# Optimization experiments

Measured on AMD Instinct MI355X. Metric: run time of the kernel, lower is better.

## Reference

```python
import jax, jax.numpy as jnp
import numpy as np

N, E, D = 50000, 800000, 128
RESIDUAL_SCALE = 1.0
EPS = 1e-5  # torch LayerNorm default eps


def _mlp_ln(h, w1, b1, w2, b2, w3, b3, g, beta):
    # MeshGraphNets MLP: Linear -> SiLU -> Linear -> SiLU -> Linear -> LayerNorm
    h = jax.nn.silu(h @ w1 + b1)
    h = jax.nn.silu(h @ w2 + b2)
    h = h @ w3 + b3
    mu = h.mean(axis=-1, keepdims=True)
    var = ((h - mu) ** 2).mean(axis=-1, keepdims=True)
    return g * (h - mu) * jax.lax.rsqrt(var + EPS) + beta


def setup_inputs() -> dict:
    key = jax.random.key(0)
    ks = jax.random.split(key, 16)

    def lin(k, fan_in, fan_out):
        bound = 1.0 / np.sqrt(fan_in)
        kw, kb = jax.random.split(k)
        w = jax.random.uniform(kw, (fan_in, fan_out), jnp.float32, -bound, bound)
        b = jax.random.uniform(kb, (fan_out,), jnp.float32, -bound, bound)
        return w, b

    x = jax.random.normal(ks[0], (N, D), jnp.float32)
    edge_attr = jax.random.normal(ks[1], (E, D), jnp.float32)
    edge_index = jax.random.randint(ks[2], (2, E), 0, N, jnp.int32)

    ew1, eb1 = lin(ks[3], 3 * D, D)
    ew2, eb2 = lin(ks[4], D, D)
    ew3, eb3 = lin(ks[5], D, D)
    e_gamma = jnp.ones((D,), jnp.float32)
    e_beta = jnp.zeros((D,), jnp.float32)

    nw1, nb1 = lin(ks[6], 2 * D, D)
    nw2, nb2 = lin(ks[7], D, D)
    nw3, nb3 = lin(ks[8], D, D)
    n_gamma = jnp.ones((D,), jnp.float32)
    n_beta = jnp.zeros((D,), jnp.float32)

    return dict(x=x, edge_attr=edge_attr, edge_index=edge_index,
                ew1=ew1, eb1=eb1, ew2=ew2, eb2=eb2, ew3=ew3, eb3=eb3,
                e_gamma=e_gamma, e_beta=e_beta,
                nw1=nw1, nb1=nb1, nw2=nw2, nb2=nb2, nw3=nw3, nb3=nb3,
                n_gamma=n_gamma, n_beta=n_beta)


def reference(x, edge_attr, edge_index,
              ew1, eb1, ew2, eb2, ew3, eb3, e_gamma, e_beta,
              nw1, nb1, nw2, nb2, nw3, nb3, n_gamma, n_beta):
    senders, receivers = edge_index[0], edge_index[1]

    # EdgeBlock: gather endpoint node features, concat with edge_attr, MLP
    edge_in = jnp.concatenate([x[senders], x[receivers], edge_attr], axis=-1)  # [E, 3D]
    edge_mlp_out = _mlp_ln(edge_in, ew1, eb1, ew2, eb2, ew3, eb3, e_gamma, e_beta)  # [E, D]

    # NodeBlock: scatter-sum edge messages to receiver nodes, concat with x, MLP
    agg = jax.ops.segment_sum(edge_mlp_out, receivers, num_segments=N)  # [N, D]
    node_in = jnp.concatenate([x, agg], axis=-1)  # [N, 2D]
    node_mlp_out = _mlp_ln(node_in, nw1, nb1, nw2, nb2, nw3, nb3, n_gamma, n_beta)

    # Residual updates
    x_new = x + RESIDUAL_SCALE * node_mlp_out

    # PairNorm (use_pairnorm=True)
    x_centered = x_new - x_new.mean(axis=0, keepdims=True)
    rms = jnp.linalg.norm(x_centered) / jnp.sqrt(jnp.float32(x_new.shape[0])) + 1e-8
    x_new = x_centered / rms

    edge_attr_new = edge_attr + RESIDUAL_SCALE * edge_mlp_out
    return x_new, edge_attr_new
```

## Files before the change

### kernel.cpp

```cpp
#include <hip/hip_runtime.h>
#include <hip/hip_bf16.h>

#define NN 50000
#define NE 800000
#define ROWB 272

typedef unsigned short u16;
typedef unsigned int u32;
typedef __attribute__((ext_vector_type(4))) float f32x4;
typedef __attribute__((ext_vector_type(8))) short short8;


__device__ __forceinline__ u16 f2b(float f){ __hip_bfloat16 h = __float2bfloat16(f); u16 u; __builtin_memcpy(&u, &h, 2); return u; }
__device__ __forceinline__ float b2f(u16 u){ __hip_bfloat16 h; __builtin_memcpy(&h, &u, 2); return __bfloat162float(h); }
__device__ __forceinline__ float siluf(float v){ return v / (1.f + __expf(-v)); }

__device__ __forceinline__ uint4 cvt8(const float* __restrict__ s){
  const float4 a = *(const float4*)s;
  const float4 b = *(const float4*)(s + 4);
  union { u16 h[8]; uint4 q; } u;
  u.h[0]=f2b(a.x); u.h[1]=f2b(a.y); u.h[2]=f2b(a.z); u.h[3]=f2b(a.w);
  u.h[4]=f2b(b.x); u.h[5]=f2b(b.y); u.h[6]=f2b(b.z); u.h[7]=f2b(b.w);
  return u.q;
}

template<int K>
__device__ __forceinline__ void gemm128(f32x4 acc[4][2], const u16* __restrict__ sA,
                                        const u16* __restrict__ wB, int wm, int wn, int lane){
  const int l15 = lane & 15, l4 = lane >> 4;
  const u16* w0 = wB + (size_t)(wn*32 + l15)*K + l4*8;
  const u16* w1 = w0 + (size_t)16*K;
  #pragma unroll
  for (int ks = 0; ks < 4; ++ks){
    const short8 b0 = *(const short8*)(w0 + ks*32);
    const short8 b1 = *(const short8*)(w1 + ks*32);
    const int kb = ks*64 + l4*16;
    short8 a[4];
    #pragma unroll
    for (int fr = 0; fr < 4; ++fr)
      a[fr] = *(const short8*)((const char*)sA + (wm*64 + fr*16 + l15)*ROWB + kb);
    #pragma unroll
    for (int fr = 0; fr < 4; ++fr){
      acc[fr][0] = __builtin_amdgcn_mfma_f32_16x16x32_bf16(a[fr], b0, acc[fr][0], 0, 0, 0);
      acc[fr][1] = __builtin_amdgcn_mfma_f32_16x16x32_bf16(a[fr], b1, acc[fr][1], 0, 0, 0);
    }
  }
}

template<int K>
__device__ __forceinline__ void gemm64(f32x4 acc[2][4], const u16* __restrict__ sA,
                                       const u16* __restrict__ wB, int wm, int wn, int lane){
  const int l15 = lane & 15, l4 = lane >> 4;
  const u16* w0 = wB + (size_t)(wn*64 + l15)*K + l4*8;
  #pragma unroll
  for (int ks = 0; ks < 4; ++ks){
    short8 b[4];
    #pragma unroll
    for (int fc = 0; fc < 4; ++fc)
      b[fc] = *(const short8*)(w0 + (size_t)fc*16*K + ks*32);
    const int kb = ks*64 + l4*16;
    short8 a[2];
    #pragma unroll
    for (int fr = 0; fr < 2; ++fr)
      a[fr] = *(const short8*)((const char*)sA + (wm*32 + fr*16 + l15)*ROWB + kb);
    #pragma unroll
    for (int fr = 0; fr < 2; ++fr)
      #pragma unroll
      for (int fc = 0; fc < 4; ++fc)
        acc[fr][fc] = __builtin_amdgcn_mfma_f32_16x16x32_bf16(a[fr], b[fc], acc[fr][fc], 0, 0, 0);
  }
}

__device__ __forceinline__ void epilogue(const f32x4 acc[4][2], const float* __restrict__ bias,
                                         u16* __restrict__ dst, int wm, int wn, int lane, bool doSilu){
  const int l15 = lane & 15, l4 = lane >> 4;
  #pragma unroll
  for (int fc = 0; fc < 2; ++fc){
    const int col = wn*32 + fc*16 + l15;
    const float bv = bias[col];
    #pragma unroll
    for (int fr = 0; fr < 4; ++fr){
      const int rbase = wm*64 + fr*16 + l4*4;
      #pragma unroll
      for (int j = 0; j < 4; ++j){
        float v = acc[fr][fc][j] + bv;
        if (doSilu) v = siluf(v);
        *(u16*)((char*)dst + (rbase + j)*ROWB + col*2) = f2b(v);
      }
    }
  }
}

__global__ __launch_bounds__(256) void prep_kernel(const float* __restrict__ w1, const float* __restrict__ w2,
                                                   const float* __restrict__ w3, const float* __restrict__ m1,
                                                   const float* __restrict__ m2, const float* __restrict__ m3,
                                                   u16* __restrict__ wt,
                                                   const float* __restrict__ x, u16* __restrict__ xB,
                                                   const int* __restrict__ eidx, int* __restrict__ cnt){
  const int i = blockIdx.x * 256 + threadIdx.x;
  if (i < 147456){
    const float* src; int K, base, off;
    if      (i < 49152)  { src = w1; K = 384; base = 0;      off = i; }
    else if (i < 65536)  { src = w2; K = 128; base = 49152;  off = i - 49152; }
    else if (i < 81920)  { src = w3; K = 128; base = 65536;  off = i - 65536; }
    else if (i < 114688) { src = m1; K = 256; base = 81920;  off = i - 81920; }
    else if (i < 131072) { src = m2; K = 128; base = 114688; off = i - 114688; }
    else                 { src = m3; K = 128; base = 131072; off = i - 131072; }
    const int k = off >> 7, n = off & 127;
    wt[base + n*K + k] = f2b(src[off]);
  }
  if (xB){
    const size_t o = (size_t)i * 8;
    *(uint4*)(xB + o) = cvt8(x + o);
  }
  atomicAdd(&cnt[eidx[NE + i]], 1);
}

__global__ __launch_bounds__(1024) void scan_kernel(const int* __restrict__ cnt, int* __restrict__ off,
                                                    int* __restrict__ cursor){
  __shared__ int s[1024];
  const int t = threadIdx.x;
  const int CH = 49;
  int sum = 0;
  for (int i = 0; i < CH; ++i){
    const int idx = t*CH + i;
    if (idx < NN) sum += cnt[idx];
  }
  s[t] = sum;
  __syncthreads();
  for (int d = 1; d < 1024; d <<= 1){
    int v = (t >= d) ? s[t - d] : 0;
    __syncthreads();
    s[t] += v;
    __syncthreads();
  }
  int run = s[t] - sum;
  for (int i = 0; i < CH; ++i){
    const int idx = t*CH + i;
    if (idx < NN){
      off[idx] = run;
      cursor[idx] = run;
      run += cnt[idx];
      if (idx == NN - 1) off[NN] = run;
    }
  }
}

__global__ __launch_bounds__(256) void scatter_kernel(const int* __restrict__ eidx, int* __restrict__ cursor,
                                                      int* __restrict__ perm, int* __restrict__ slot){
  const int i = blockIdx.x * 256 + threadIdx.x;
  if (i < NE){
    const int pos = atomicAdd(&cursor[eidx[NE + i]], 1);
    perm[pos] = i;
    slot[i] = pos;
  }
}

__global__ __launch_bounds__(256, 4) void pre_kernel(const float* __restrict__ x, const u16* __restrict__ xB,
                                                     const u16* __restrict__ wt, u16* __restrict__ Pab){
  __shared__ u16 sX[64*136];
  const int t = threadIdx.x;
  const int nBase = blockIdx.x * 64;
  const int lane = t & 63, wid = t >> 6;
  const int wm = wid >> 1, wn = wid & 1;
  const int chunk = t & 15, r0 = t >> 4;

  #pragma unroll
  for (int p = 0; p < 4; ++p){
    const int row = r0 + p*16;
    const int node = nBase + row;
    uint4 v = {0u, 0u, 0u, 0u};
    if (node < NN){
      if (xB) v = *(const uint4*)(xB + (size_t)node*128 + chunk*8);
      else    v = cvt8(x + (size_t)node*128 + chunk*8);
    }
    *(uint4*)((char*)sX + row*ROWB + chunk*16) = v;
  }
  __syncthreads();

  const f32x4 z4 = {0.f, 0.f, 0.f, 0.f};
  const int l15 = lane & 15, l4 = lane >> 4;
  #pragma unroll
  for (int half = 0; half < 2; ++half){
    f32x4 acc[2][4];
    #pragma unroll
    for (int fr = 0; fr < 2; ++fr)
      #pragma unroll
      for (int fc = 0; fc < 4; ++fc) acc[fr][fc] = z4;
    gemm64<384>(acc, sX, wt + half*128, wm, wn, lane);
    #pragma unroll
    for (int fc = 0; fc < 4; ++fc){
      const int col = wn*64 + fc*16 + l15;
      #pragma unroll
      for (int fr = 0; fr < 2; ++fr){
        const int rbase = wm*32 + fr*16 + l4*4;
        #pragma unroll
        for (int j = 0; j < 4; ++j){
          const int node = nBase + rbase + j;
          if (node < NN) Pab[(size_t)node*256 + half*128 + col] = f2b(acc[fr][fc][j]);
        }
      }
    }
  }
}

__global__ __launch_bounds__(512, 4) void edge_kernel(
    const float* __restrict__ ea, const int* __restrict__ eidx,
    const u16* __restrict__ wt, const u16* __restrict__ Pab,
    const float* __restrict__ b1, const float* __restrict__ b2,
    const float* __restrict__ b3, const float* __restrict__ gma, const float* __restrict__ bta,
    const int* __restrict__ slot, float* __restrict__ outE, u16* __restrict__ oBuf)
{
  __shared__ u16 sA[128*136];
  __shared__ float sMeta[640];
  __shared__ int sIdx[256];
  __shared__ int sSlot[128];
  const int t = threadIdx.x;
  const size_t eBase = (size_t)blockIdx.x * 128;

  if (t < 128){
    sIdx[t]       = eidx[eBase + t];
    sIdx[t + 128] = eidx[(size_t)NE + eBase + t];
    sSlot[t]      = slot[eBase + t];
    sMeta[t]       = b1[t];
    sMeta[t + 128] = b2[t];
    sMeta[t + 256] = b3[t];
    sMeta[t + 384] = gma[t];
    sMeta[t + 512] = bta[t];
  }
  __syncthreads();

  const int lane = t & 63, wid = t >> 6;
  const int wm = wid >> 2, wn = wid & 3;
  const int chunk = t & 15, r0 = t >> 4;
  const int l15 = lane & 15, l4 = lane >> 4;

  #pragma unroll
  for (int p = 0; p < 4; ++p){
    const int row = r0 + p*32;
    const int sn = sIdx[row], rn = sIdx[row + 128];
    const uint4 qa = *(const uint4*)(Pab + (size_t)sn*256 + chunk*8);
    const uint4 qb = *(const uint4*)(Pab + (size_t)rn*256 + 128 + chunk*8);
    const u16* pa = (const u16*)&qa;
    const u16* pb = (const u16*)&qb;
    union { u16 h[8]; uint4 q; } u;
    #pragma unroll
    for (int j = 0; j < 8; ++j) u.h[j] = f2b(b2f(pa[j]) + b2f(pb[j]));
    *(uint4*)((char*)sA + row*ROWB + chunk*16) = u.q;
  }
  __syncthreads();

  f32x4 acc[4][2];
  #pragma unroll
  for (int fr = 0; fr < 4; ++fr)
    #pragma unroll
    for (int fc = 0; fc < 2; ++fc){
      const int col = wn*32 + fc*16 + l15;
      #pragma unroll
      for (int j = 0; j < 4; ++j)
        acc[fr][fc][j] = b2f(*(const u16*)((const char*)sA + (wm*64 + fr*16 + l4*4 + j)*ROWB + col*2));
    }
  __syncthreads();

  uint4 eaQ[4];
  #pragma unroll
  for (int p = 0; p < 4; ++p){
    const int row = r0 + p*32;
    uint4 v = cvt8(ea + ((eBase + row)*128 + chunk*8));
    eaQ[p] = v;
    *(uint4*)((char*)sA + row*ROWB + chunk*16) = v;
  }
  __syncthreads();
  gemm128<384>(acc, sA, wt + 256, wm, wn, lane);
  __syncthreads();
  epilogue(acc, sMeta + 0, sA, wm, wn, lane, true);
  __syncthreads();
  const f32x4 z4 = {0.f, 0.f, 0.f, 0.f};
  #pragma unroll
  for (int fr = 0; fr < 4; ++fr){ acc[fr][0] = z4; acc[fr][1] = z4; }
  gemm128<128>(acc, sA, wt + 49152, wm, wn, lane);
  __syncthreads();
  epilogue(acc, sMeta + 128, sA, wm, wn, lane, true);
  __syncthreads();
  #pragma unroll
  for (int fr = 0; fr < 4; ++fr){ acc[fr][0] = z4; acc[fr][1] = z4; }
  gemm128<128>(acc, sA, wt + 65536, wm, wn, lane);
  __syncthreads();
  epilogue(acc, sMeta + 256, sA, wm, wn, lane, false);
  __syncthreads();

  {
    #pragma unroll
    for (int p = 0; p < 4; ++p){
      const int row = r0 + p*32;
      uint4 q = *(const uint4*)((const char*)sA + row*ROWB + chunk*16);
      const u16* pu = (const u16*)&q;
      float h[8];
      #pragma unroll
      for (int j = 0; j < 8; ++j) h[j] = b2f(pu[j]);
      float s = 0.f;
      #pragma unroll
      for (int j = 0; j < 8; ++j) s += h[j];
      s += __shfl_xor(s, 1); s += __shfl_xor(s, 2); s += __shfl_xor(s, 4); s += __shfl_xor(s, 8);
      const float mu = s * (1.f/128.f);
      float ss = 0.f;
      #pragma unroll
      for (int j = 0; j < 8; ++j){ const float d = h[j] - mu; ss += d*d; }
      ss += __shfl_xor(ss, 1); ss += __shfl_xor(ss, 2); ss += __shfl_xor(ss, 4); ss += __shfl_xor(ss, 8);
      const float rs = rsqrtf(fmaxf(ss*(1.f/128.f), 0.f) + 1e-5f);
      const size_t e = eBase + row;
      const u16* ep = (const u16*)&eaQ[p];
      alignas(16) float orow[8];
      alignas(16) u16 obf[8];
      #pragma unroll
      for (int j = 0; j < 8; ++j){
        const int col = chunk*8 + j;
        const float o = sMeta[384 + col]*(h[j] - mu)*rs + sMeta[512 + col];
        orow[j] = b2f(ep[j]) + o;
        obf[j] = f2b(o);
      }
      float* dst = outE + e*128 + chunk*8;
      *(float4*)dst       = ((const float4*)orow)[0];
      *(float4*)(dst + 4) = ((const float4*)orow)[1];
      if (oBuf) *(uint4*)(oBuf + (size_t)sSlot[row]*128 + chunk*8) = *(const uint4*)obf;
    }
  }
}

__global__ __launch_bounds__(256) void agg_f_kernel(const float* __restrict__ outE, const float* __restrict__ ea,
                                                    const int* __restrict__ off, const int* __restrict__ perm,
                                                    float* __restrict__ agg){
  const int node = blockIdx.x * 4 + (threadIdx.x >> 6);
  const int lane = threadIdx.x & 63;
  if (node >= NN) return;
  const int s = off[node], e = off[node + 1];
  float a0 = 0.f, a1 = 0.f;
  for (int i = s; i < e; ++i){
    const size_t r = (size_t)perm[i] * 128;
    a0 += outE[r + lane]      - ea[r + lane];
    a1 += outE[r + 64 + lane] - ea[r + 64 + lane];
  }
  agg[(size_t)node*128 + lane]      = a0;
  agg[(size_t)node*128 + 64 + lane] = a1;
}

__global__ __launch_bounds__(512, 4) void node_kernel(
    const float* __restrict__ x, const float* __restrict__ aggF,
    const u16* __restrict__ oBuf, const int* __restrict__ off,
    const u16* __restrict__ wt,
    const float* __restrict__ b1, const float* __restrict__ b2, const float* __restrict__ b3,
    const float* __restrict__ gma, const float* __restrict__ bta,
    float* __restrict__ outX, float* __restrict__ stats)
{
  __shared__ u16 sA[128*136];
  __shared__ float sMeta[640];
  __shared__ float sCol[128];
  __shared__ float sSq;
  const int t = threadIdx.x;
  const int nBase = blockIdx.x * 128;

  if (t < 128){
    sMeta[t]       = b1[t];
    sMeta[t + 128] = b2[t];
    sMeta[t + 256] = b3[t];
    sMeta[t + 384] = gma[t];
    sMeta[t + 512] = bta[t];
    sCol[t] = 0.f;
  }
  if (t == 0) sSq = 0.f;
  __syncthreads();

  const int lane = t & 63, wid = t >> 6;
  const int wm = wid >> 2, wn = wid & 3;
  const int chunk = t & 15, r0 = t >> 4;

  const f32x4 z4 = {0.f, 0.f, 0.f, 0.f};
  f32x4 acc[4][2];
  #pragma unroll
  for (int fr = 0; fr < 4; ++fr){ acc[fr][0] = z4; acc[fr][1] = z4; }

  for (int kc = 0; kc < 2; ++kc){
    #pragma unroll
    for (int p = 0; p < 4; ++p){
      const int row = r0 + p*32;
      const int node = nBase + row;
      uint4 v = {0u, 0u, 0u, 0u};
      if (node < NN){
        if (kc == 0){
          v = cvt8(x + (size_t)node*128 + chunk*8);
        } else if (oBuf){
          float a[8] = {0.f,0.f,0.f,0.f,0.f,0.f,0.f,0.f};
          const int s0 = off[node], e0 = off[node + 1];
          for (int i = s0; i < e0; ++i){
            uint4 q = *(const uint4*)(oBuf + (size_t)i*128 + chunk*8);
            const u16* pu = (const u16*)&q;
            #pragma unroll
            for (int j = 0; j < 8; ++j) a[j] += b2f(pu[j]);
          }
          union { u16 h[8]; uint4 q; } u;
          #pragma unroll
          for (int j = 0; j < 8; ++j) u.h[j] = f2b(a[j]);
          v = u.q;
        } else {
          v = cvt8(aggF + (size_t)node*128 + chunk*8);
        }
      }
      *(uint4*)((char*)sA + row*ROWB + chunk*16) = v;
    }
    __syncthreads();
    gemm128<256>(acc, sA, wt + 81920 + kc*128, wm, wn, lane);
    __syncthreads();
  }
  epilogue(acc, sMeta + 0, sA, wm, wn, lane, true);
  __syncthreads();
  #pragma unroll
  for (int fr = 0; fr < 4; ++fr){ acc[fr][0] = z4; acc[fr][1] = z4; }
  gemm128<128>(acc, sA, wt + 114688, wm, wn, lane);
  __syncthreads();
  epilogue(acc, sMeta + 128, sA, wm, wn, lane, true);
  __syncthreads();
  #pragma unroll
  for (int fr = 0; fr < 4; ++fr){ acc[fr][0] = z4; acc[fr][1] = z4; }
  gemm128<128>(acc, sA, wt + 131072, wm, wn, lane);
  __syncthreads();
  epilogue(acc, sMeta + 256, sA, wm, wn, lane, false);
  __syncthreads();

  {
    const int row = t >> 2, part = t & 3;
    const int node = nBase + row;
    float v[32];
    #pragma unroll
    for (int c = 0; c < 4; ++c){
      uint4 q = *(const uint4*)((const char*)sA + row*ROWB + part*64 + c*16);
      const u16* pu = (const u16*)&q;
      #pragma unroll
      for (int j = 0; j < 8; ++j) v[c*8 + j] = b2f(pu[j]);
    }
    float s = 0.f;
    #pragma unroll
    for (int i = 0; i < 32; ++i) s += v[i];
    s += __shfl_xor(s, 1);  s += __shfl_xor(s, 2);
    const float mu = s * (1.f/128.f);
    float ss = 0.f;
    #pragma unroll
    for (int i = 0; i < 32; ++i){ const float d = v[i] - mu; ss += d*d; }
    ss += __shfl_xor(ss, 1);  ss += __shfl_xor(ss, 2);
    const float rs = rsqrtf(fmaxf(ss*(1.f/128.f), 0.f) + 1e-5f);
    float lssq = 0.f;
    if (node < NN){
      const float* xRow = x + (size_t)node*128 + part*32;
      alignas(16) float orow[32];
      #pragma unroll
      for (int i = 0; i < 32; ++i){
        const int col = part*32 + i;
        const float o = sMeta[384 + col]*(v[i] - mu)*rs + sMeta[512 + col];
        const float res = xRow[i] + o;
        orow[i] = res;
        atomicAdd(&sCol[col], res);
        lssq += res*res;
      }
      float* dst = outX + (size_t)node*128 + part*32;
      #pragma unroll
      for (int c = 0; c < 8; ++c) *(float4*)(dst + c*4) = ((const float4*)orow)[c];
    }
    #pragma unroll
    for (int m = 1; m < 64; m <<= 1) lssq += __shfl_xor(lssq, m);
    if (lane == 0) atomicAdd(&sSq, lssq);
  }
  __syncthreads();
  if (t < 128) atomicAdd(&stats[t], sCol[t]);
  if (t == 0)  atomicAdd(&stats[128], sSq);
}

__global__ __launch_bounds__(256) void pairnorm_kernel(float* __restrict__ xOut, const float* __restrict__ stats){
  __shared__ float sMean[128];
  __shared__ float sP2[2];
  __shared__ float sInv;
  const int t = threadIdx.x;
  float m2 = 0.f;
  if (t < 128){
    const float mean = stats[t] * (1.f / (float)NN);
    sMean[t] = mean;
    m2 = mean * mean;
  }
  #pragma unroll
  for (int m = 1; m < 64; m <<= 1) m2 += __shfl_xor(m2, m);
  if ((t & 63) == 0 && t < 128) sP2[t >> 6] = m2;
  __syncthreads();
  if (t == 0){
    float ssc = stats[128] - (float)NN * (sP2[0] + sP2[1]);
    ssc = fmaxf(ssc, 0.f);
    const float rms = sqrtf(ssc * (1.f / (float)NN)) + 1e-8f;
    sInv = 1.f / rms;
  }
  __syncthreads();
  const size_t base = ((size_t)blockIdx.x * 256 + t) * 4;
  const int col = (int)(base & 127);
  float4 q = *(float4*)(xOut + base);
  const float inv = sInv;
  q.x = (q.x - sMean[col])     * inv;
  q.y = (q.y - sMean[col + 1]) * inv;
  q.z = (q.z - sMean[col + 2]) * inv;
  q.w = (q.w - sMean[col + 3]) * inv;
  *(float4*)(xOut + base) = q;
}

extern "C" void kernel_launch(void* const* d_in, const int* in_sizes, int n_in,
                              void* d_out, int out_size, void* d_ws, size_t ws_size,
                              hipStream_t stream){
  (void)in_sizes; (void)n_in; (void)out_size;
  const float* x    = (const float*)d_in[0];
  const float* ea   = (const float*)d_in[1];
  const int*   eidx = (const int*)d_in[2];
  const float* ew1  = (const float*)d_in[3];
  const float* eb1  = (const float*)d_in[4];
  const float* ew2  = (const float*)d_in[5];
  const float* eb2  = (const float*)d_in[6];
  const float* ew3  = (const float*)d_in[7];
  const float* eb3  = (const float*)d_in[8];
  const float* eg   = (const float*)d_in[9];
  const float* ebt  = (const float*)d_in[10];
  const float* nw1  = (const float*)d_in[11];
  const float* nb1  = (const float*)d_in[12];
  const float* nw2  = (const float*)d_in[13];
  const float* nb2  = (const float*)d_in[14];
  const float* nw3  = (const float*)d_in[15];
  const float* nb3  = (const float*)d_in[16];
  const float* ng   = (const float*)d_in[17];
  const float* nbt  = (const float*)d_in[18];

  u16*   wt     = (u16*)d_ws;
  float* stats  = (float*)((char*)d_ws + 294912);
  int*   cnt    = (int*)((char*)d_ws + 297216);
  int*   off    = (int*)((char*)d_ws + 497408);
  int*   cursor = (int*)((char*)d_ws + 697600);
  int*   perm   = (int*)((char*)d_ws + 897792);
  int*   slot   = (int*)((char*)d_ws + 4097792);
  const bool useO = ws_size >= (7297792ull + (size_t)NE * 128 * 2);
  const bool useX = ws_size >= (7297792ull + (size_t)NE * 128 * 2 + (size_t)NN * 128 * 2);
  u16*   oBuf   = useO ? (u16*)((char*)d_ws + 7297792) : (u16*)nullptr;
  u16*   xB     = useX ? (u16*)((char*)d_ws + 7297792 + (size_t)NE * 128 * 2) : (u16*)nullptr;
  float* outX   = (float*)d_out;
  u16*   Pab    = (u16*)d_out;
  float* outE   = outX + (size_t)NN * 128;

  hipMemsetAsync(stats, 0, 2048, stream);
  hipMemsetAsync(cnt, 0, NN * sizeof(int), stream);
  prep_kernel<<<3125, 256, 0, stream>>>(ew1, ew2, ew3, nw1, nw2, nw3, wt, x, xB, eidx, cnt);
  scan_kernel<<<1, 1024, 0, stream>>>(cnt, off, cursor);
  scatter_kernel<<<3125, 256, 0, stream>>>(eidx, cursor, perm, slot);
  pre_kernel<<<782, 256, 0, stream>>>(x, xB, wt, Pab);
  edge_kernel<<<6250, 512, 0, stream>>>(ea, eidx, wt, Pab, eb1, eb2, eb3, eg, ebt, slot, outE, oBuf);
  if (!useO) agg_f_kernel<<<12500, 256, 0, stream>>>(outE, ea, off, perm, outX);
  node_kernel<<<391, 512, 0, stream>>>(x, outX, oBuf, off, wt, nb1, nb2, nb3, ng, nbt, outX, stats);
  pairnorm_kernel<<<6250, 256, 0, stream>>>(outX, stats);
}
```

Before: 763.0 us.

## Process two 128-edge tiles per block with interleaved double-buffered stages

Each edge block now handles 256 edges as two 128-row tiles in separate LDS buffers. The gather, GEMM, epilogue and LayerNorm stages of the two tiles are interleaved so one tile's loads or math can overlap the other's, and the per-block setup is amortised over twice the edges. In exchange LDS use doubles, register pressure rises with two accumulator sets, and the grid is halved, which can lower occupancy under the launch bound of 512 threads and 4 blocks.

```diff
diff --git a/kernel.cpp b/kernel.cpp
--- a/kernel.cpp
+++ b/kernel.cpp
@@ -88,6 +88,89 @@
         *(u16*)((char*)dst + (rbase + j)*ROWB + col*2) = f2b(v);
       }
     }
+  }
+}
+
+__device__ __forceinline__ void stageP(u16* __restrict__ sT, const int* __restrict__ snd,
+                                       const int* __restrict__ rcv, const u16* __restrict__ Pab,
+                                       int r0, int chunk){
+  #pragma unroll
+  for (int p = 0; p < 4; ++p){
+    const int row = r0 + p*32;
+    const int sn = snd[row], rn = rcv[row];
+    const uint4 qa = *(const uint4*)(Pab + (size_t)sn*256 + chunk*8);
+    const uint4 qb = *(const uint4*)(Pab + (size_t)rn*256 + 128 + chunk*8);
+    const u16* pa = (const u16*)&qa;
+    const u16* pb = (const u16*)&qb;
+    union { u16 h[8]; uint4 q; } u;
+    #pragma unroll
+    for (int j = 0; j < 8; ++j) u.h[j] = f2b(b2f(pa[j]) + b2f(pb[j]));
+    *(uint4*)((char*)sT + row*ROWB + chunk*16) = u.q;
+  }
+}
+
+__device__ __forceinline__ void seedAcc(f32x4 acc[4][2], const u16* __restrict__ sT,
+                                        int wm, int wn, int lane){
+  const int l15 = lane & 15, l4 = lane >> 4;
+  #pragma unroll
+  for (int fr = 0; fr < 4; ++fr)
+    #pragma unroll
+    for (int fc = 0; fc < 2; ++fc){
+      const int col = wn*32 + fc*16 + l15;
+      #pragma unroll
+      for (int j = 0; j < 4; ++j)
+        acc[fr][fc][j] = b2f(*(const u16*)((const char*)sT + (wm*64 + fr*16 + l4*4 + j)*ROWB + col*2));
+    }
+}
+
+__device__ __forceinline__ void stageE(u16* __restrict__ sT, uint4* __restrict__ eaQ,
+                                       const float* __restrict__ ea, size_t eb, int r0, int chunk){
+  #pragma unroll
+  for (int p = 0; p < 4; ++p){
+    const int row = r0 + p*32;
+    uint4 v = cvt8(ea + ((eb + row)*128 + chunk*8));
+    eaQ[p] = v;
+    *(uint4*)((char*)sT + row*ROWB + chunk*16) = v;
+  }
+}
+
+__device__ __forceinline__ void lnOut(const u16* __restrict__ sT, const uint4* __restrict__ eaQ,
+                                      const float* __restrict__ sMeta, const int* __restrict__ slt,
+                                      size_t eb, int r0, int chunk,
+                                      float* __restrict__ outE, u16* __restrict__ oBuf){
+  #pragma unroll
+  for (int p = 0; p < 4; ++p){
+    const int row = r0 + p*32;
+    uint4 q = *(const uint4*)((const char*)sT + row*ROWB + chunk*16);
+    const u16* pu = (const u16*)&q;
+    float h[8];
+    #pragma unroll
+    for (int j = 0; j < 8; ++j) h[j] = b2f(pu[j]);
+    float s = 0.f;
+    #pragma unroll
+    for (int j = 0; j < 8; ++j) s += h[j];
+    s += __shfl_xor(s, 1); s += __shfl_xor(s, 2); s += __shfl_xor(s, 4); s += __shfl_xor(s, 8);
+    const float mu = s * (1.f/128.f);
+    float ss = 0.f;
+    #pragma unroll
+    for (int j = 0; j < 8; ++j){ const float d = h[j] - mu; ss += d*d; }
+    ss += __shfl_xor(ss, 1); ss += __shfl_xor(ss, 2); ss += __shfl_xor(ss, 4); ss += __shfl_xor(ss, 8);
+    const float rs = rsqrtf(fmaxf(ss*(1.f/128.f), 0.f) + 1e-5f);
+    const size_t e = eb + row;
+    const u16* ep = (const u16*)&eaQ[p];
+    alignas(16) float orow[8];
+    alignas(16) u16 obf[8];
+    #pragma unroll
+    for (int j = 0; j < 8; ++j){
+      const int col = chunk*8 + j;
+      const float o = sMeta[384 + col]*(h[j] - mu)*rs + sMeta[512 + col];
+      orow[j] = b2f(ep[j]) + o;
+      obf[j] = f2b(o);
+    }
+    float* dst = outE + e*128 + chunk*8;
+    *(float4*)dst       = ((const float4*)orow)[0];
+    *(float4*)(dst + 4) = ((const float4*)orow)[1];
+    if (oBuf) *(uint4*)(oBuf + (size_t)slt[row]*128 + chunk*8) = *(const uint4*)obf;
   }
 }
 
@@ -211,120 +294,78 @@
     const float* __restrict__ b3, const float* __restrict__ gma, const float* __restrict__ bta,
     const int* __restrict__ slot, float* __restrict__ outE, u16* __restrict__ oBuf)
 {
-  __shared__ u16 sA[128*136];
+  __shared__ u16 sTA[128*136];
+  __shared__ u16 sTB[128*136];
   __shared__ float sMeta[640];
-  __shared__ int sIdx[256];
-  __shared__ int sSlot[128];
+  __shared__ int sSnd[256];
+  __shared__ int sRcv[256];
+  __shared__ int sSlt[256];
   const int t = threadIdx.x;
-  const size_t eBase = (size_t)blockIdx.x * 128;
-
-  if (t < 128){
-    sIdx[t]       = eidx[eBase + t];
-    sIdx[t + 128] = eidx[(size_t)NE + eBase + t];
-    sSlot[t]      = slot[eBase + t];
-    sMeta[t]       = b1[t];
-    sMeta[t + 128] = b2[t];
-    sMeta[t + 256] = b3[t];
-    sMeta[t + 384] = gma[t];
-    sMeta[t + 512] = bta[t];
+  const size_t eBase = (size_t)blockIdx.x * 256;
+
+  if (t < 256){
+    sSnd[t] = eidx[eBase + t];
+    sRcv[t] = eidx[(size_t)NE + eBase + t];
+    sSlt[t] = slot[eBase + t];
+  } else {
+    const int m = t - 256;
+    if (m < 128){
+      sMeta[m]       = b1[m];
+      sMeta[m + 128] = b2[m];
+      sMeta[m + 256] = b3[m];
+      sMeta[m + 384] = gma[m];
+      sMeta[m + 512] = bta[m];
+    }
   }
   __syncthreads();
 
   const int lane = t & 63, wid = t >> 6;
   const int wm = wid >> 2, wn = wid & 3;
   const int chunk = t & 15, r0 = t >> 4;
-  const int l15 = lane & 15, l4 = lane >> 4;
-
-  #pragma unroll
-  for (int p = 0; p < 4; ++p){
-    const int row = r0 + p*32;
-    const int sn = sIdx[row], rn = sIdx[row + 128];
-    const uint4 qa = *(const uint4*)(Pab + (size_t)sn*256 + chunk*8);
-    const uint4 qb = *(const uint4*)(Pab + (size_t)rn*256 + 128 + chunk*8);
-    const u16* pa = (const u16*)&qa;
-    const u16* pb = (const u16*)&qb;
-    union { u16 h[8]; uint4 q; } u;
-    #pragma unroll
-    for (int j = 0; j < 8; ++j) u.h[j] = f2b(b2f(pa[j]) + b2f(pb[j]));
-    *(uint4*)((char*)sA + row*ROWB + chunk*16) = u.q;
-  }
-  __syncthreads();
-
-  f32x4 acc[4][2];
-  #pragma unroll
-  for (int fr = 0; fr < 4; ++fr)
-    #pragma unroll
-    for (int fc = 0; fc < 2; ++fc){
-      const int col = wn*32 + fc*16 + l15;
-      #pragma unroll
-      for (int j = 0; j < 4; ++j)
-        acc[fr][fc][j] = b2f(*(const u16*)((const char*)sA + (wm*64 + fr*16 + l4*4 + j)*ROWB + col*2));
-    }
-  __syncthreads();
-
-  uint4 eaQ[4];
-  #pragma unroll
-  for (int p = 0; p < 4; ++p){
-    const int row = r0 + p*32;
-    uint4 v = cvt8(ea + ((eBase + row)*128 + chunk*8));
-    eaQ[p] = v;
-    *(uint4*)((char*)sA + row*ROWB + chunk*16) = v;
-  }
-  __syncthreads();
-  gemm128<384>(acc, sA, wt + 256, wm, wn, lane);
-  __syncthreads();
-  epilogue(acc, sMeta + 0, sA, wm, wn, lane, true);
-  __syncthreads();
+  const size_t ebA = eBase, ebB = eBase + 128;
+
   const f32x4 z4 = {0.f, 0.f, 0.f, 0.f};
-  #pragma unroll
-  for (int fr = 0; fr < 4; ++fr){ acc[fr][0] = z4; acc[fr][1] = z4; }
-  gemm128<128>(acc, sA, wt + 49152, wm, wn, lane);
-  __syncthreads();
-  epilogue(acc, sMeta + 128, sA, wm, wn, lane, true);
-  __syncthreads();
-  #pragma unroll
-  for (int fr = 0; fr < 4; ++fr){ acc[fr][0] = z4; acc[fr][1] = z4; }
-  gemm128<128>(acc, sA, wt + 65536, wm, wn, lane);
-  __syncthreads();
-  epilogue(acc, sMeta + 256, sA, wm, wn, lane, false);
-  __syncthreads();
-
-  {
-    #pragma unroll
-    for (int p = 0; p < 4; ++p){
-      const int row = r0 + p*32;
-      uint4 q = *(const uint4*)((const char*)sA + row*ROWB + chunk*16);
-      const u16* pu = (const u16*)&q;
-      float h[8];
-      #pragma unroll
-      for (int j = 0; j < 8; ++j) h[j] = b2f(pu[j]);
-      float s = 0.f;
-      #pragma unroll
-      for (int j = 0; j < 8; ++j) s += h[j];
-      s += __shfl_xor(s, 1); s += __shfl_xor(s, 2); s += __shfl_xor(s, 4); s += __shfl_xor(s, 8);
-      const float mu = s * (1.f/128.f);
-      float ss = 0.f;
-      #pragma unroll
-      for (int j = 0; j < 8; ++j){ const float d = h[j] - mu; ss += d*d; }
-      ss += __shfl_xor(ss, 1); ss += __shfl_xor(ss, 2); ss += __shfl_xor(ss, 4); ss += __shfl_xor(ss, 8);
-      const float rs = rsqrtf(fmaxf(ss*(1.f/128.f), 0.f) + 1e-5f);
-      const size_t e = eBase + row;
-      const u16* ep = (const u16*)&eaQ[p];
-      alignas(16) float orow[8];
-      alignas(16) u16 obf[8];
-      #pragma unroll
-      for (int j = 0; j < 8; ++j){
-        const int col = chunk*8 + j;
-        const float o = sMeta[384 + col]*(h[j] - mu)*rs + sMeta[512 + col];
-        orow[j] = b2f(ep[j]) + o;
-        obf[j] = f2b(o);
-      }
-      float* dst = outE + e*128 + chunk*8;
-      *(float4*)dst       = ((const float4*)orow)[0];
-      *(float4*)(dst + 4) = ((const float4*)orow)[1];
-      if (oBuf) *(uint4*)(oBuf + (size_t)sSlot[row]*128 + chunk*8) = *(const uint4*)obf;
-    }
-  }
+  f32x4 accA[4][2], accB[4][2];
+  uint4 eaQA[4], eaQB[4];
+
+  stageP(sTA, sSnd, sRcv, Pab, r0, chunk);
+  __syncthreads();
+  stageP(sTB, sSnd + 128, sRcv + 128, Pab, r0, chunk);
+  seedAcc(accA, sTA, wm, wn, lane);
+  __syncthreads();
+  stageE(sTA, eaQA, ea, ebA, r0, chunk);
+  seedAcc(accB, sTB, wm, wn, lane);
+  __syncthreads();
+  stageE(sTB, eaQB, ea, ebB, r0, chunk);
+  gemm128<384>(accA, sTA, wt + 256, wm, wn, lane);
+  __syncthreads();
+  epilogue(accA, sMeta + 0, sTA, wm, wn, lane, true);
+  gemm128<384>(accB, sTB, wt + 256, wm, wn, lane);
+  __syncthreads();
+  epilogue(accB, sMeta + 0, sTB, wm, wn, lane, true);
+  #pragma unroll
+  for (int fr = 0; fr < 4; ++fr){ accA[fr][0] = z4; accA[fr][1] = z4; }
+  gemm128<128>(accA, sTA, wt + 49152, wm, wn, lane);
+  __syncthreads();
+  epilogue(accA, sMeta + 128, sTA, wm, wn, lane, true);
+  #pragma unroll
+  for (int fr = 0; fr < 4; ++fr){ accB[fr][0] = z4; accB[fr][1] = z4; }
+  gemm128<128>(accB, sTB, wt + 49152, wm, wn, lane);
+  __syncthreads();
+  epilogue(accB, sMeta + 128, sTB, wm, wn, lane, true);
+  #pragma unroll
+  for (int fr = 0; fr < 4; ++fr){ accA[fr][0] = z4; accA[fr][1] = z4; }
+  gemm128<128>(accA, sTA, wt + 65536, wm, wn, lane);
+  __syncthreads();
+  epilogue(accA, sMeta + 256, sTA, wm, wn, lane, false);
+  #pragma unroll
+  for (int fr = 0; fr < 4; ++fr){ accB[fr][0] = z4; accB[fr][1] = z4; }
+  gemm128<128>(accB, sTB, wt + 65536, wm, wn, lane);
+  __syncthreads();
+  epilogue(accB, sMeta + 256, sTB, wm, wn, lane, false);
+  lnOut(sTA, eaQA, sMeta, sSlt, ebA, r0, chunk, outE, oBuf);
+  __syncthreads();
+  lnOut(sTB, eaQB, sMeta, sSlt + 128, ebB, r0, chunk, outE, oBuf);
 }
 
 __global__ __launch_bounds__(256) void agg_f_kernel(const float* __restrict__ outE, const float* __restrict__ ea,
@@ -551,7 +592,7 @@
   scan_kernel<<<1, 1024, 0, stream>>>(cnt, off, cursor);
   scatter_kernel<<<3125, 256, 0, stream>>>(eidx, cursor, perm, slot);
   pre_kernel<<<782, 256, 0, stream>>>(x, xB, wt, Pab);
-  edge_kernel<<<6250, 512, 0, stream>>>(ea, eidx, wt, Pab, eb1, eb2, eb3, eg, ebt, slot, outE, oBuf);
+  edge_kernel<<<3125, 512, 0, stream>>>(ea, eidx, wt, Pab, eb1, eb2, eb3, eg, ebt, slot, outE, oBuf);
   if (!useO) agg_f_kernel<<<12500, 256, 0, stream>>>(outE, ea, off, perm, outX);
   node_kernel<<<391, 512, 0, stream>>>(x, outX, oBuf, off, wt, nb1, nb2, nb3, ng, nbt, outX, stats);
   pairnorm_kernel<<<6250, 256, 0, stream>>>(outX, stats);
```

Measured after the change: 872.7 us. +14.4%, slower.
